# Optimization experiments

Measured on AMD Instinct MI355X. Metric: run time of the kernel, lower is better.

The kernel has to match this reference:

```python
import jax, jax.numpy as jnp
import numpy as np

T, B, IN, HID, NL = 256, 256, 64, 512, 2
LS = HID // NL  # per-layer hidden size of GRUCellStack


def setup_inputs() -> dict:
    key = jax.random.key(0)
    ks = jax.random.split(key, 9)
    w = lambda k, shape: (jax.random.normal(k, shape, jnp.float32) * 0.05)
    return {
        "obs": jax.random.normal(ks[0], (T, B, IN), jnp.float32),
        "reset": jax.random.randint(ks[1], (T, B), 0, 2).astype(bool),
        "h": jnp.zeros((B, HID), jnp.float32),
        "W_lin": w(ks[2], (HID, IN)),
        "b_lin": jnp.zeros((HID,), jnp.float32),
        "w_ih0": w(ks[3], (3 * LS, HID)),
        "w_hh0": w(ks[4], (3 * LS, LS)),
        "b_ih0": jnp.zeros((3 * LS,), jnp.float32),
        "b_hh0": jnp.zeros((3 * LS,), jnp.float32),
        "w_ih1": w(ks[5], (3 * LS, LS)),
        "w_hh1": w(ks[6], (3 * LS, LS)),
        "b_ih1": jnp.zeros((3 * LS,), jnp.float32),
        "b_hh1": jnp.zeros((3 * LS,), jnp.float32),
    }


def _gru_cell(i_gates, h, w_hh, b_hh):
    # PyTorch nn.GRUCell math; i_gates = x @ w_ih.T + b_ih precomputed.
    h_gates = h @ w_hh.T + b_hh
    ir, iz, in_ = jnp.split(i_gates, 3, axis=-1)
    hr, hz, hn = jnp.split(h_gates, 3, axis=-1)
    r = jax.nn.sigmoid(ir + hr)
    z = jax.nn.sigmoid(iz + hz)
    n = jnp.tanh(in_ + r * hn)
    return (1.0 - z) * n + z * h


def reference(obs, reset, h, W_lin, b_lin, w_ih0, w_hh0, b_ih0, b_hh0,
              w_ih1, w_hh1, b_ih1, b_hh1):
    # embed all timesteps at once: [T,B,HID]
    x = obs.astype(jnp.float32) @ W_lin.T + b_lin
    # layer-0 input-side gates depend only on x -> precompute: [T,B,3*LS]
    ig0 = x @ w_ih0.T + b_ih0
    mask = (~reset).astype(jnp.float32)[..., None]  # [T,B,1]

    def step(hc, inp):
        ig0_t, m_t = inp
        hc = hc * m_t                      # reset masking of full stacked state
        h0, h1 = jnp.split(hc, 2, axis=-1)  # per-layer states [B,LS]
        h0n = _gru_cell(ig0_t, h0, w_hh0, b_hh0)
        ig1 = h0n @ w_ih1.T + b_ih1
        h1n = _gru_cell(ig1, h1, w_hh1, b_hh1)
        hn = jnp.concatenate([h0n, h1n], axis=-1)  # [B,HID]
        return hn, hn

    _, states_h = jax.lax.scan(step, h, (ig0, mask))
    return states_h  # [T,B,HID]
```

## Files before the change

### kernel.cpp

```cpp
#include <hip/hip_runtime.h>

#define T_    256
#define B_    256
#define IN_   64
#define HID_  512
#define LS_   256
#define G3_   768
#define TBS_  32
#define MBT_  64
#define WP_   264
#define FSTRIDE_ 128

typedef short bf16x8v __attribute__((ext_vector_type(8)));
typedef float f32x4  __attribute__((ext_vector_type(4)));
typedef unsigned long long u64;

#define MFMA_B16(A, B, C) __builtin_amdgcn_mfma_f32_16x16x32_bf16(A, B, C, 0, 0, 0)

__device__ __forceinline__ unsigned short f2bf(float f) {
  union { float f; unsigned u; } v; v.f = f;
  unsigned r = v.u + 0x7fffu + ((v.u >> 16) & 1u);
  return (unsigned short)(r >> 16);
}
__device__ __forceinline__ float sigm(float x) { return 1.0f / (1.0f + __expf(-x)); }
__device__ __forceinline__ float tanh_f(float x) {
  x = fminf(fmaxf(x, -15.0f), 15.0f);
  float e = __expf(-2.0f * x);
  return (1.0f - e) / (1.0f + e);
}

__device__ __forceinline__ void st2_coh(unsigned short* p, unsigned short v) {
  __hip_atomic_store(p, v, __ATOMIC_RELAXED, __HIP_MEMORY_SCOPE_AGENT);
}
__device__ __forceinline__ bf16x8v ld16_coh(const unsigned short* p) {
  union { u64 q[2]; bf16x8v v; } u;
  u.q[0] = __hip_atomic_load((const u64*)p,     __ATOMIC_RELAXED, __HIP_MEMORY_SCOPE_AGENT);
  u.q[1] = __hip_atomic_load((const u64*)(p+4), __ATOMIC_RELAXED, __HIP_MEMORY_SCOPE_AGENT);
  return u.v;
}

__global__ void prep_conv(const float* __restrict__ whh0, const float* __restrict__ wih1,
                          const float* __restrict__ whh1, const unsigned char* __restrict__ rst,
                          unsigned short* __restrict__ dst, int* __restrict__ flagp,
                          int* __restrict__ flags) {
  const int idx = blockIdx.x * blockDim.x + threadIdx.x;
  const int N1 = G3_ * LS_;
  if (idx < 3 * N1) {
    float v;
    if (idx < N1)            v = whh0[idx];
    else if (idx < 2 * N1)   v = wih1[idx - N1];
    else                     v = whh1[idx - 2 * N1];
    dst[idx] = f2bf(v);
  }
  if (blockIdx.x == 1 && threadIdx.x < 32) {
    flags[threadIdx.x * FSTRIDE_] = 0;
  }
  if (blockIdx.x == 0) {
    __shared__ int f;
    if (threadIdx.x == 0) f = 0;
    __syncthreads();
    int any = 0;
    for (int i = 0; i < 8; ++i) {
      int off = threadIdx.x * 8 + i;
      if ((off & 3) && rst[off]) any = 1;
    }
    if (any) atomicOr(&f, 1);
    __syncthreads();
    if (threadIdx.x == 0) *flagp = f;
  }
}

__global__ void prep_wc(const float* __restrict__ W_lin, const float* __restrict__ b_lin,
                        const float* __restrict__ w_ih0, const float* __restrict__ b_ih0,
                        unsigned short* __restrict__ wc, float* __restrict__ bc) {
  const int n = blockIdx.x;
  const int i = threadIdx.x;
  const float* wrow = w_ih0 + (size_t)n * HID_;
  float acc = 0.f;
  for (int h = 0; h < HID_; ++h) acc += wrow[h] * W_lin[h * IN_ + i];
  wc[n * IN_ + i] = f2bf(acc);
  float pb = 0.f;
  for (int h = i; h < HID_; h += 64) pb += wrow[h] * b_lin[h];
  __shared__ float red[64];
  red[i] = pb;
  __syncthreads();
  if (i == 0) {
    float s = 0.f;
    for (int k = 0; k < 64; ++k) s += red[k];
    bc[n] = s + b_ih0[n];
  }
}

__global__ __launch_bounds__(512, 2) void gru_main(
    const float* __restrict__ obs, const unsigned char* __restrict__ rst,
    const float* __restrict__ h_init,
    const unsigned short* __restrict__ wc,
    const unsigned short* __restrict__ whh0g,
    const unsigned short* __restrict__ wih1g, const unsigned short* __restrict__ whh1g,
    const float* __restrict__ bcp, const float* __restrict__ bhh0,
    const float* __restrict__ bih1, const float* __restrict__ bhh1,
    const int* __restrict__ flagp, int* __restrict__ flag0,
    unsigned short* __restrict__ hx0, unsigned short* __restrict__ hx1,
    float* __restrict__ out) {

  __shared__ __align__(16) unsigned short wlds[3 * 96 * WP_];
  __shared__ int s_sm[64];
  __shared__ int s_start_sh;

  const int tid  = threadIdx.x;
  const int lane = tid & 63;
  const int wave = tid >> 6;
  const int l15  = lane & 15;
  const int quad = lane >> 4;
  const int mt   = wave & 3;
  const int c16  = (wave >> 2) * 16;

  const int x  = blockIdx.x;
  const int cx = x & 7, m8 = x >> 3;
  const int j  = m8 & 7;
  const int team = cx * 4 + (m8 >> 3);
  const int bg = team & 3, tc = team >> 2;
  const int b0 = bg * MBT_, t0 = tc * TBS_;

  int* f0 = flag0 + team * FSTRIDE_;

  const int flag = *flagp;
#define RVAL(i) (rst[flag ? (i) : ((i) << 2)] != 0)

#pragma unroll
  for (int q = 0; q < 3; ++q) {
    const unsigned short* src = (q == 0) ? whh0g : (q == 1) ? wih1g : whh1g;
    for (int cid = tid; cid < 96 * 32; cid += 512) {
      int lr = cid >> 5, off8 = (cid & 31) * 8;
      int g = lr >> 5, cc = lr & 31;
      int grow = (g << 8) + (j << 5) + cc;
      *(f32x4*)&wlds[(q * 96 + lr) * WP_ + off8] =
          *(const f32x4*)&src[(size_t)grow * 256 + off8];
    }
  }

  const int colg = j * 32 + c16 + l15;
  const float b0r = bcp[colg] + bhh0[colg];
  const float b0z = bcp[256 + colg] + bhh0[256 + colg];
  const float b0i = bcp[512 + colg];
  const float b0h = bhh0[512 + colg];
  const float b1r = bih1[colg] + bhh1[colg];
  const float b1z = bih1[256 + colg] + bhh1[256 + colg];
  const float b1i = bih1[512 + colg];
  const float b1h = bhh1[512 + colg];

  if (tid < 64) {
    int s = 0;
    for (int tt = t0; tt >= 1; --tt) {
      if (RVAL(tt * B_ + b0 + tid)) { s = tt; break; }
    }
    s_sm[tid] = s;
  }
  __syncthreads();
  if (tid == 0) {
    int s = s_sm[0];
    for (int k = 1; k < 64; ++k) s = s < s_sm[k] ? s : s_sm[k];
    s_start_sh = s;
  }
  __syncthreads();
  const int s_start = s_start_sh;

  bf16x8v h0A[8], h1A[8];
  const bf16x8v z8 = {0, 0, 0, 0, 0, 0, 0, 0};
#pragma unroll
  for (int kc = 0; kc < 8; ++kc) { h0A[kc] = z8; h1A[kc] = z8; }
  float h0v[4] = {0.f, 0.f, 0.f, 0.f}, h1v[4] = {0.f, 0.f, 0.f, 0.f};
  if (s_start == 0) {
    const float* hrow = h_init + (size_t)(b0 + mt * 16 + l15) * HID_;
#pragma unroll
    for (int kc = 0; kc < 8; ++kc) {
      f32x4 u0 = *(const f32x4*)(hrow + kc * 32 + quad * 8);
      f32x4 u1 = *(const f32x4*)(hrow + kc * 32 + quad * 8 + 4);
      f32x4 v0 = *(const f32x4*)(hrow + 256 + kc * 32 + quad * 8);
      f32x4 v1 = *(const f32x4*)(hrow + 256 + kc * 32 + quad * 8 + 4);
      bf16x8v a, b;
#pragma unroll
      for (int e = 0; e < 4; ++e) {
        a[e] = (short)f2bf(u0[e]); a[4 + e] = (short)f2bf(u1[e]);
        b[e] = (short)f2bf(v0[e]); b[4 + e] = (short)f2bf(v1[e]);
      }
      h0A[kc] = a; h1A[kc] = b;
    }
#pragma unroll
    for (int r = 0; r < 4; ++r) {
      const int m = mt * 16 + quad * 4 + r;
      h0v[r] = h_init[(size_t)(b0 + m) * HID_ + colg];
      h1v[r] = h_init[(size_t)(b0 + m) * HID_ + 256 + colg];
    }
  }

  const unsigned short* wR0 = &wlds[(0 * 96 + 0 * 32 + c16 + l15) * WP_];
  const unsigned short* wZ0 = &wlds[(0 * 96 + 1 * 32 + c16 + l15) * WP_];
  const unsigned short* wN0 = &wlds[(0 * 96 + 2 * 32 + c16 + l15) * WP_];
  const unsigned short* iR1 = &wlds[(1 * 96 + 0 * 32 + c16 + l15) * WP_];
  const unsigned short* iZ1 = &wlds[(1 * 96 + 1 * 32 + c16 + l15) * WP_];
  const unsigned short* iN1 = &wlds[(1 * 96 + 2 * 32 + c16 + l15) * WP_];
  const unsigned short* hR1 = &wlds[(2 * 96 + 0 * 32 + c16 + l15) * WP_];
  const unsigned short* hZ1 = &wlds[(2 * 96 + 1 * 32 + c16 + l15) * WP_];
  const unsigned short* hN1 = &wlds[(2 * 96 + 2 * 32 + c16 + l15) * WP_];

  f32x4 ou0a, ou0b, ou1a, ou1b;
  {
    const float* po = obs + ((size_t)s_start * B_ + b0 + mt * 16 + l15) * IN_;
    ou0a = __builtin_nontemporal_load((const f32x4*)(po + quad * 8));
    ou0b = __builtin_nontemporal_load((const f32x4*)(po + quad * 8 + 4));
    ou1a = __builtin_nontemporal_load((const f32x4*)(po + 32 + quad * 8));
    ou1b = __builtin_nontemporal_load((const f32x4*)(po + 32 + quad * 8 + 4));
  }

  for (int t = s_start; t < t0 + TBS_; ++t) {
    const int  kk = t - s_start + 1;
    const bool wr = (t >= t0);
    const bool rs0 = RVAL(t * B_ + b0 + mt * 16 + l15);
    bool rse[4];
#pragma unroll
    for (int r = 0; r < 4; ++r) rse[r] = RVAL(t * B_ + b0 + mt * 16 + quad * 4 + r);

    f32x4 ar = {0.f, 0.f, 0.f, 0.f}, az = ar, ani = ar, anh = ar;
    {
#pragma unroll
      for (int kc = 0; kc < 2; ++kc) {
        f32x4 u0 = kc ? ou1a : ou0a;
        f32x4 u1 = kc ? ou1b : ou0b;
        bf16x8v oA;
#pragma unroll
        for (int e = 0; e < 4; ++e) { oA[e] = (short)f2bf(u0[e]); oA[4 + e] = (short)f2bf(u1[e]); }
        const size_t wo = (size_t)colg * 64 + kc * 32 + quad * 8;
        bf16x8v br = *(const bf16x8v*)&wc[wo];
        bf16x8v bz = *(const bf16x8v*)&wc[wo + (size_t)256 * 64];
        bf16x8v bn = *(const bf16x8v*)&wc[wo + (size_t)512 * 64];
        ar  = MFMA_B16(oA, br, ar);
        az  = MFMA_B16(oA, bz, az);
        ani = MFMA_B16(oA, bn, ani);
      }
    }
#pragma unroll
    for (int kc = 0; kc < 8; ++kc) {
      bf16x8v am = rs0 ? z8 : h0A[kc];
      const int o = kc * 32 + quad * 8;
      ar  = MFMA_B16(am, *(const bf16x8v*)&wR0[o], ar);
      az  = MFMA_B16(am, *(const bf16x8v*)&wZ0[o], az);
      anh = MFMA_B16(am, *(const bf16x8v*)&wN0[o], anh);
    }
    {
      unsigned short* hw = hx0 + ((size_t)team * 2 + (kk & 1)) * (MBT_ * 256);
#pragma unroll
      for (int r = 0; r < 4; ++r) {
        const int m = mt * 16 + quad * 4 + r;
        float rr = sigm(ar[r] + b0r);
        float zz = sigm(az[r] + b0z);
        float nn = tanh_f(ani[r] + b0i + rr * (anh[r] + b0h));
        float hp = rse[r] ? 0.f : h0v[r];
        float hv = (1.f - zz) * nn + zz * hp;
        h0v[r] = hv;
        st2_coh(hw + m * 256 + colg, f2bf(hv));
      }
    }
    __syncthreads();
    if (tid == 0) {
      __hip_atomic_fetch_add(f0, 1, __ATOMIC_RELAXED, __HIP_MEMORY_SCOPE_AGENT);
      int cap = 0;
      while (__hip_atomic_load(f0, __ATOMIC_RELAXED, __HIP_MEMORY_SCOPE_AGENT)
                 < 8 * kk && cap < (1 << 16)) { __builtin_amdgcn_s_sleep(2); ++cap; }
    }
    __syncthreads();
    {
      const unsigned short* hr0 =
          hx0 + ((size_t)team * 2 + (kk & 1)) * (MBT_ * 256) + (mt * 16 + l15) * 256;
#pragma unroll
      for (int kc = 0; kc < 8; ++kc)
        h0A[kc] = ld16_coh(hr0 + kc * 32 + quad * 8);
      if (kk >= 2) {
        const unsigned short* hr1 =
            hx1 + ((size_t)team * 2 + ((kk - 1) & 1)) * (MBT_ * 256) + (mt * 16 + l15) * 256;
#pragma unroll
        for (int kc = 0; kc < 8; ++kc)
          h1A[kc] = ld16_coh(hr1 + kc * 32 + quad * 8);
      }
    }
    if (wr) {
#pragma unroll
      for (int r = 0; r < 4; ++r) {
        const int m = mt * 16 + quad * 4 + r;
        __builtin_nontemporal_store(h0v[r], &out[((size_t)t * B_ + b0 + m) * HID_ + colg]);
      }
    }
    if (t - 1 >= t0) {
#pragma unroll
      for (int r = 0; r < 4; ++r) {
        const int m = mt * 16 + quad * 4 + r;
        __builtin_nontemporal_store(h1v[r],
            &out[((size_t)(t - 1) * B_ + b0 + m) * HID_ + 256 + colg]);
      }
    }
    {
      const int tn = (t + 1 < t0 + TBS_) ? t + 1 : t;
      const float* po = obs + ((size_t)tn * B_ + b0 + mt * 16 + l15) * IN_;
      ou0a = __builtin_nontemporal_load((const f32x4*)(po + quad * 8));
      ou0b = __builtin_nontemporal_load((const f32x4*)(po + quad * 8 + 4));
      ou1a = __builtin_nontemporal_load((const f32x4*)(po + 32 + quad * 8));
      ou1b = __builtin_nontemporal_load((const f32x4*)(po + 32 + quad * 8 + 4));
    }

    ar = (f32x4){0.f, 0.f, 0.f, 0.f}; az = ar; ani = ar; anh = ar;
#pragma unroll
    for (int kc = 0; kc < 8; ++kc) {
      bf16x8v ai_ = h0A[kc];
      bf16x8v am  = rs0 ? z8 : h1A[kc];
      const int o = kc * 32 + quad * 8;
      ar  = MFMA_B16(ai_, *(const bf16x8v*)&iR1[o], ar);
      az  = MFMA_B16(ai_, *(const bf16x8v*)&iZ1[o], az);
      ani = MFMA_B16(ai_, *(const bf16x8v*)&iN1[o], ani);
      ar  = MFMA_B16(am, *(const bf16x8v*)&hR1[o], ar);
      az  = MFMA_B16(am, *(const bf16x8v*)&hZ1[o], az);
      anh = MFMA_B16(am, *(const bf16x8v*)&hN1[o], anh);
    }
    {
      unsigned short* hw = hx1 + ((size_t)team * 2 + (kk & 1)) * (MBT_ * 256);
#pragma unroll
      for (int r = 0; r < 4; ++r) {
        const int m = mt * 16 + quad * 4 + r;
        float rr = sigm(ar[r] + b1r);
        float zz = sigm(az[r] + b1z);
        float nn = tanh_f(ani[r] + b1i + rr * (anh[r] + b1h));
        float hp = rse[r] ? 0.f : h1v[r];
        float hv = (1.f - zz) * nn + zz * hp;
        h1v[r] = hv;
        st2_coh(hw + m * 256 + colg, f2bf(hv));
      }
    }
  }
  {
    const int tl = t0 + TBS_ - 1;
#pragma unroll
    for (int r = 0; r < 4; ++r) {
      const int m = mt * 16 + quad * 4 + r;
      __builtin_nontemporal_store(h1v[r],
          &out[((size_t)tl * B_ + b0 + m) * HID_ + 256 + colg]);
    }
  }
#undef RVAL
}

extern "C" void kernel_launch(void* const* d_in, const int* in_sizes, int n_in,
                              void* d_out, int out_size, void* d_ws, size_t ws_size,
                              hipStream_t stream) {
  const float* obs    = (const float*)d_in[0];
  const unsigned char* rst = (const unsigned char*)d_in[1];
  const float* h_init = (const float*)d_in[2];
  const float* W_lin  = (const float*)d_in[3];
  const float* b_lin  = (const float*)d_in[4];
  const float* w_ih0  = (const float*)d_in[5];
  const float* w_hh0  = (const float*)d_in[6];
  const float* b_ih0  = (const float*)d_in[7];
  const float* b_hh0  = (const float*)d_in[8];
  const float* w_ih1  = (const float*)d_in[9];
  const float* w_hh1  = (const float*)d_in[10];
  const float* b_ih1  = (const float*)d_in[11];
  const float* b_hh1  = (const float*)d_in[12];

  char* w = (char*)d_ws;
  unsigned short* wcp   = (unsigned short*)(w);
  unsigned short* whh0b = (unsigned short*)(w + 98304);
  unsigned short* wih1b = (unsigned short*)(w + 491520);
  unsigned short* whh1b = (unsigned short*)(w + 884736);
  float*          bcp   = (float*)(w + 1277952);
  int*            flagp = (int*)(w + 1281024);
  int*            flags = (int*)(w + 1281088);
  unsigned short* hx0   = (unsigned short*)(w + 1310720);
  unsigned short* hx1   = (unsigned short*)(w + 1310720 + 2097152);

  prep_conv<<<1152, 512, 0, stream>>>(w_hh0, w_ih1, w_hh1, rst, whh0b, flagp, flags);
  prep_wc<<<768, 64, 0, stream>>>(W_lin, b_lin, w_ih0, b_ih0, wcp, bcp);
  gru_main<<<256, 512, 0, stream>>>(obs, rst, h_init, wcp, whh0b, wih1b, whh1b,
                                    bcp, b_hh0, b_ih1, b_hh1, flagp,
                                    flags, hx0, hx1, (float*)d_out);
}
```

Measured before the change: 658.2 us.

## Rebalance GRU teams to 128-row batches with 16-step chunks, merge prep kernels

Each team now owns 128 batch rows over 16 time steps instead of 64 rows over 32 steps. Each wave covers one 16-row M tile and both 16-column groups, so every h-row A fragment is reused across two column groups. The intent is to shorten each team's sequential time chunk and its warm-up replay. The cost is more accumulators and registers per wave and larger exchange buffers. The two preprocessing kernels are merged into one launch, and the bias reduction now uses wave shuffles.

```diff
diff --git a/kernel.cpp b/kernel.cpp
--- a/kernel.cpp
+++ b/kernel.cpp
@@ -6,8 +6,8 @@
 #define HID_  512
 #define LS_   256
 #define G3_   768
-#define TBS_  32
-#define MBT_  64
+#define TBS_  16
+#define MBT_  128
 #define WP_   264
 #define FSTRIDE_ 128
 
@@ -39,55 +39,51 @@
   return u.v;
 }
 
-__global__ void prep_conv(const float* __restrict__ whh0, const float* __restrict__ wih1,
-                          const float* __restrict__ whh1, const unsigned char* __restrict__ rst,
-                          unsigned short* __restrict__ dst, int* __restrict__ flagp,
-                          int* __restrict__ flags) {
-  const int idx = blockIdx.x * blockDim.x + threadIdx.x;
-  const int N1 = G3_ * LS_;
-  if (idx < 3 * N1) {
-    float v;
-    if (idx < N1)            v = whh0[idx];
-    else if (idx < 2 * N1)   v = wih1[idx - N1];
-    else                     v = whh1[idx - 2 * N1];
-    dst[idx] = f2bf(v);
-  }
-  if (blockIdx.x == 1 && threadIdx.x < 32) {
-    flags[threadIdx.x * FSTRIDE_] = 0;
-  }
-  if (blockIdx.x == 0) {
-    __shared__ int f;
-    if (threadIdx.x == 0) f = 0;
-    __syncthreads();
-    int any = 0;
-    for (int i = 0; i < 8; ++i) {
-      int off = threadIdx.x * 8 + i;
-      if ((off & 3) && rst[off]) any = 1;
-    }
-    if (any) atomicOr(&f, 1);
-    __syncthreads();
-    if (threadIdx.x == 0) *flagp = f;
-  }
-}
-
-__global__ void prep_wc(const float* __restrict__ W_lin, const float* __restrict__ b_lin,
-                        const float* __restrict__ w_ih0, const float* __restrict__ b_ih0,
-                        unsigned short* __restrict__ wc, float* __restrict__ bc) {
-  const int n = blockIdx.x;
-  const int i = threadIdx.x;
-  const float* wrow = w_ih0 + (size_t)n * HID_;
-  float acc = 0.f;
-  for (int h = 0; h < HID_; ++h) acc += wrow[h] * W_lin[h * IN_ + i];
-  wc[n * IN_ + i] = f2bf(acc);
-  float pb = 0.f;
-  for (int h = i; h < HID_; h += 64) pb += wrow[h] * b_lin[h];
-  __shared__ float red[64];
-  red[i] = pb;
-  __syncthreads();
-  if (i == 0) {
-    float s = 0.f;
-    for (int k = 0; k < 64; ++k) s += red[k];
-    bc[n] = s + b_ih0[n];
+__global__ void prep_all(const float* __restrict__ whh0, const float* __restrict__ wih1,
+                         const float* __restrict__ whh1, const unsigned char* __restrict__ rst,
+                         const float* __restrict__ W_lin, const float* __restrict__ b_lin,
+                         const float* __restrict__ w_ih0, const float* __restrict__ b_ih0,
+                         unsigned short* __restrict__ dst, unsigned short* __restrict__ wc,
+                         float* __restrict__ bc, int* __restrict__ flagp,
+                         int* __restrict__ flags) {
+  const int bx = blockIdx.x;
+  const int tid = threadIdx.x;
+  if (bx < 1152) {
+    const int idx = bx * 512 + tid;
+    const int N1 = G3_ * LS_;
+    if (idx < 3 * N1) {
+      float v;
+      if (idx < N1)            v = whh0[idx];
+      else if (idx < 2 * N1)   v = wih1[idx - N1];
+      else                     v = whh1[idx - 2 * N1];
+      dst[idx] = f2bf(v);
+    }
+    if (bx == 1 && tid < 32) flags[tid * FSTRIDE_] = 0;
+    if (bx == 0) {
+      __shared__ int f;
+      if (tid == 0) f = 0;
+      __syncthreads();
+      int any = 0;
+      for (int i = 0; i < 8; ++i) {
+        int off = tid * 8 + i;
+        if ((off & 3) && rst[off]) any = 1;
+      }
+      if (any) atomicOr(&f, 1);
+      __syncthreads();
+      if (tid == 0) *flagp = f;
+    }
+  } else {
+    const int n = (bx - 1152) * 8 + (tid >> 6);
+    const int i = tid & 63;
+    const float* wrow = w_ih0 + (size_t)n * HID_;
+    float acc = 0.f;
+    for (int h = 0; h < HID_; ++h) acc += wrow[h] * W_lin[h * IN_ + i];
+    wc[n * IN_ + i] = f2bf(acc);
+    float pb = 0.f;
+    for (int h = i; h < HID_; h += 64) pb += wrow[h] * b_lin[h];
+#pragma unroll
+    for (int off = 32; off > 0; off >>= 1) pb += __shfl_down(pb, off);
+    if (i == 0) bc[n] = pb + b_ih0[n];
   }
 }
 
@@ -104,22 +100,20 @@
     float* __restrict__ out) {
 
   __shared__ __align__(16) unsigned short wlds[3 * 96 * WP_];
-  __shared__ int s_sm[64];
+  __shared__ int s_sm[128];
   __shared__ int s_start_sh;
 
   const int tid  = threadIdx.x;
   const int lane = tid & 63;
-  const int wave = tid >> 6;
+  const int w    = tid >> 6;
   const int l15  = lane & 15;
   const int quad = lane >> 4;
-  const int mt   = wave & 3;
-  const int c16  = (wave >> 2) * 16;
 
   const int x  = blockIdx.x;
   const int cx = x & 7, m8 = x >> 3;
   const int j  = m8 & 7;
   const int team = cx * 4 + (m8 >> 3);
-  const int bg = team & 3, tc = team >> 2;
+  const int bg = team & 1, tc = team >> 1;
   const int b0 = bg * MBT_, t0 = tc * TBS_;
 
   int* f0 = flag0 + team * FSTRIDE_;
@@ -139,17 +133,21 @@
     }
   }
 
-  const int colg = j * 32 + c16 + l15;
-  const float b0r = bcp[colg] + bhh0[colg];
-  const float b0z = bcp[256 + colg] + bhh0[256 + colg];
-  const float b0i = bcp[512 + colg];
-  const float b0h = bhh0[512 + colg];
-  const float b1r = bih1[colg] + bhh1[colg];
-  const float b1z = bih1[256 + colg] + bhh1[256 + colg];
-  const float b1i = bih1[512 + colg];
-  const float b1h = bhh1[512 + colg];
-
-  if (tid < 64) {
+  float b0r[2], b0z[2], b0i[2], b0h[2], b1r[2], b1z[2], b1i[2], b1h[2];
+#pragma unroll
+  for (int cg = 0; cg < 2; ++cg) {
+    const int c = j * 32 + cg * 16 + l15;
+    b0r[cg] = bcp[c] + bhh0[c];
+    b0z[cg] = bcp[256 + c] + bhh0[256 + c];
+    b0i[cg] = bcp[512 + c];
+    b0h[cg] = bhh0[512 + c];
+    b1r[cg] = bih1[c] + bhh1[c];
+    b1z[cg] = bih1[256 + c] + bhh1[256 + c];
+    b1i[cg] = bih1[512 + c];
+    b1h[cg] = bhh1[512 + c];
+  }
+
+  if (tid < 128) {
     int s = 0;
     for (int tt = t0; tt >= 1; --tt) {
       if (RVAL(tt * B_ + b0 + tid)) { s = tt; break; }
@@ -159,7 +157,7 @@
   __syncthreads();
   if (tid == 0) {
     int s = s_sm[0];
-    for (int k = 1; k < 64; ++k) s = s < s_sm[k] ? s : s_sm[k];
+    for (int k = 1; k < 128; ++k) s = s < s_sm[k] ? s : s_sm[k];
     s_start_sh = s;
   }
   __syncthreads();
@@ -169,9 +167,13 @@
   const bf16x8v z8 = {0, 0, 0, 0, 0, 0, 0, 0};
 #pragma unroll
   for (int kc = 0; kc < 8; ++kc) { h0A[kc] = z8; h1A[kc] = z8; }
-  float h0v[4] = {0.f, 0.f, 0.f, 0.f}, h1v[4] = {0.f, 0.f, 0.f, 0.f};
+  float h0v[2][4] = {{0.f}}, h1v[2][4] = {{0.f}};
+#pragma unroll
+  for (int cg = 0; cg < 2; ++cg)
+#pragma unroll
+    for (int r = 0; r < 4; ++r) { h0v[cg][r] = 0.f; h1v[cg][r] = 0.f; }
   if (s_start == 0) {
-    const float* hrow = h_init + (size_t)(b0 + mt * 16 + l15) * HID_;
+    const float* hrow = h_init + (size_t)(b0 + w * 16 + l15) * HID_;
 #pragma unroll
     for (int kc = 0; kc < 8; ++kc) {
       f32x4 u0 = *(const f32x4*)(hrow + kc * 32 + quad * 8);
@@ -187,26 +189,30 @@
       h0A[kc] = a; h1A[kc] = b;
     }
 #pragma unroll
-    for (int r = 0; r < 4; ++r) {
-      const int m = mt * 16 + quad * 4 + r;
-      h0v[r] = h_init[(size_t)(b0 + m) * HID_ + colg];
-      h1v[r] = h_init[(size_t)(b0 + m) * HID_ + 256 + colg];
-    }
-  }
-
-  const unsigned short* wR0 = &wlds[(0 * 96 + 0 * 32 + c16 + l15) * WP_];
-  const unsigned short* wZ0 = &wlds[(0 * 96 + 1 * 32 + c16 + l15) * WP_];
-  const unsigned short* wN0 = &wlds[(0 * 96 + 2 * 32 + c16 + l15) * WP_];
-  const unsigned short* iR1 = &wlds[(1 * 96 + 0 * 32 + c16 + l15) * WP_];
-  const unsigned short* iZ1 = &wlds[(1 * 96 + 1 * 32 + c16 + l15) * WP_];
-  const unsigned short* iN1 = &wlds[(1 * 96 + 2 * 32 + c16 + l15) * WP_];
-  const unsigned short* hR1 = &wlds[(2 * 96 + 0 * 32 + c16 + l15) * WP_];
-  const unsigned short* hZ1 = &wlds[(2 * 96 + 1 * 32 + c16 + l15) * WP_];
-  const unsigned short* hN1 = &wlds[(2 * 96 + 2 * 32 + c16 + l15) * WP_];
+    for (int cg = 0; cg < 2; ++cg)
+#pragma unroll
+      for (int r = 0; r < 4; ++r) {
+        const int m = w * 16 + quad * 4 + r;
+        const int c = j * 32 + cg * 16 + l15;
+        h0v[cg][r] = h_init[(size_t)(b0 + m) * HID_ + c];
+        h1v[cg][r] = h_init[(size_t)(b0 + m) * HID_ + 256 + c];
+      }
+  }
+
+  const unsigned short* wR0 = &wlds[(0 * 96 + 0 * 32 + l15) * WP_];
+  const unsigned short* wZ0 = &wlds[(0 * 96 + 1 * 32 + l15) * WP_];
+  const unsigned short* wN0 = &wlds[(0 * 96 + 2 * 32 + l15) * WP_];
+  const unsigned short* iR1 = &wlds[(1 * 96 + 0 * 32 + l15) * WP_];
+  const unsigned short* iZ1 = &wlds[(1 * 96 + 1 * 32 + l15) * WP_];
+  const unsigned short* iN1 = &wlds[(1 * 96 + 2 * 32 + l15) * WP_];
+  const unsigned short* hR1 = &wlds[(2 * 96 + 0 * 32 + l15) * WP_];
+  const unsigned short* hZ1 = &wlds[(2 * 96 + 1 * 32 + l15) * WP_];
+  const unsigned short* hN1 = &wlds[(2 * 96 + 2 * 32 + l15) * WP_];
+#define CGO_ (16 * WP_)
 
   f32x4 ou0a, ou0b, ou1a, ou1b;
   {
-    const float* po = obs + ((size_t)s_start * B_ + b0 + mt * 16 + l15) * IN_;
+    const float* po = obs + ((size_t)s_start * B_ + b0 + w * 16 + l15) * IN_;
     ou0a = __builtin_nontemporal_load((const f32x4*)(po + quad * 8));
     ou0b = __builtin_nontemporal_load((const f32x4*)(po + quad * 8 + 4));
     ou1a = __builtin_nontemporal_load((const f32x4*)(po + 32 + quad * 8));
@@ -216,12 +222,17 @@
   for (int t = s_start; t < t0 + TBS_; ++t) {
     const int  kk = t - s_start + 1;
     const bool wr = (t >= t0);
-    const bool rs0 = RVAL(t * B_ + b0 + mt * 16 + l15);
+    const bool rs0 = RVAL(t * B_ + b0 + w * 16 + l15);
     bool rse[4];
 #pragma unroll
-    for (int r = 0; r < 4; ++r) rse[r] = RVAL(t * B_ + b0 + mt * 16 + quad * 4 + r);
-
-    f32x4 ar = {0.f, 0.f, 0.f, 0.f}, az = ar, ani = ar, anh = ar;
+    for (int r = 0; r < 4; ++r) rse[r] = RVAL(t * B_ + b0 + w * 16 + quad * 4 + r);
+
+    f32x4 ar[2], az[2], ani[2], anh[2];
+#pragma unroll
+    for (int cg = 0; cg < 2; ++cg) {
+      ar[cg] = (f32x4){0.f, 0.f, 0.f, 0.f};
+      az[cg] = ar[cg]; ani[cg] = ar[cg]; anh[cg] = ar[cg];
+    }
     {
 #pragma unroll
       for (int kc = 0; kc < 2; ++kc) {
@@ -230,36 +241,44 @@
         bf16x8v oA;
 #pragma unroll
         for (int e = 0; e < 4; ++e) { oA[e] = (short)f2bf(u0[e]); oA[4 + e] = (short)f2bf(u1[e]); }
-        const size_t wo = (size_t)colg * 64 + kc * 32 + quad * 8;
-        bf16x8v br = *(const bf16x8v*)&wc[wo];
-        bf16x8v bz = *(const bf16x8v*)&wc[wo + (size_t)256 * 64];
-        bf16x8v bn = *(const bf16x8v*)&wc[wo + (size_t)512 * 64];
-        ar  = MFMA_B16(oA, br, ar);
-        az  = MFMA_B16(oA, bz, az);
-        ani = MFMA_B16(oA, bn, ani);
+#pragma unroll
+        for (int cg = 0; cg < 2; ++cg) {
+          const size_t wo = (size_t)(j * 32 + cg * 16 + l15) * 64 + kc * 32 + quad * 8;
+          bf16x8v br = *(const bf16x8v*)&wc[wo];
+          bf16x8v bz = *(const bf16x8v*)&wc[wo + (size_t)256 * 64];
+          bf16x8v bn = *(const bf16x8v*)&wc[wo + (size_t)512 * 64];
+          ar[cg]  = MFMA_B16(oA, br, ar[cg]);
+          az[cg]  = MFMA_B16(oA, bz, az[cg]);
+          ani[cg] = MFMA_B16(oA, bn, ani[cg]);
+        }
       }
     }
 #pragma unroll
     for (int kc = 0; kc < 8; ++kc) {
       bf16x8v am = rs0 ? z8 : h0A[kc];
       const int o = kc * 32 + quad * 8;
-      ar  = MFMA_B16(am, *(const bf16x8v*)&wR0[o], ar);
-      az  = MFMA_B16(am, *(const bf16x8v*)&wZ0[o], az);
-      anh = MFMA_B16(am, *(const bf16x8v*)&wN0[o], anh);
+#pragma unroll
+      for (int cg = 0; cg < 2; ++cg) {
+        ar[cg]  = MFMA_B16(am, *(const bf16x8v*)&wR0[o + cg * CGO_], ar[cg]);
+        az[cg]  = MFMA_B16(am, *(const bf16x8v*)&wZ0[o + cg * CGO_], az[cg]);
+        anh[cg] = MFMA_B16(am, *(const bf16x8v*)&wN0[o + cg * CGO_], anh[cg]);
+      }
     }
     {
       unsigned short* hw = hx0 + ((size_t)team * 2 + (kk & 1)) * (MBT_ * 256);
 #pragma unroll
-      for (int r = 0; r < 4; ++r) {
-        const int m = mt * 16 + quad * 4 + r;
-        float rr = sigm(ar[r] + b0r);
-        float zz = sigm(az[r] + b0z);
-        float nn = tanh_f(ani[r] + b0i + rr * (anh[r] + b0h));
-        float hp = rse[r] ? 0.f : h0v[r];
-        float hv = (1.f - zz) * nn + zz * hp;
-        h0v[r] = hv;
-        st2_coh(hw + m * 256 + colg, f2bf(hv));
-      }
+      for (int cg = 0; cg < 2; ++cg)
+#pragma unroll
+        for (int r = 0; r < 4; ++r) {
+          const int m = w * 16 + quad * 4 + r;
+          float rr = sigm(ar[cg][r] + b0r[cg]);
+          float zz = sigm(az[cg][r] + b0z[cg]);
+          float nn = tanh_f(ani[cg][r] + b0i[cg] + rr * (anh[cg][r] + b0h[cg]));
+          float hp = rse[r] ? 0.f : h0v[cg][r];
+          float hv = (1.f - zz) * nn + zz * hp;
+          h0v[cg][r] = hv;
+          st2_coh(hw + m * 256 + j * 32 + cg * 16 + l15, f2bf(hv));
+        }
     }
     __syncthreads();
     if (tid == 0) {
@@ -271,13 +290,13 @@
     __syncthreads();
     {
       const unsigned short* hr0 =
-          hx0 + ((size_t)team * 2 + (kk & 1)) * (MBT_ * 256) + (mt * 16 + l15) * 256;
+          hx0 + ((size_t)team * 2 + (kk & 1)) * (MBT_ * 256) + (w * 16 + l15) * 256;
 #pragma unroll
       for (int kc = 0; kc < 8; ++kc)
         h0A[kc] = ld16_coh(hr0 + kc * 32 + quad * 8);
       if (kk >= 2) {
         const unsigned short* hr1 =
-            hx1 + ((size_t)team * 2 + ((kk - 1) & 1)) * (MBT_ * 256) + (mt * 16 + l15) * 256;
+            hx1 + ((size_t)team * 2 + ((kk - 1) & 1)) * (MBT_ * 256) + (w * 16 + l15) * 256;
 #pragma unroll
         for (int kc = 0; kc < 8; ++kc)
           h1A[kc] = ld16_coh(hr1 + kc * 32 + quad * 8);
@@ -285,66 +304,83 @@
     }
     if (wr) {
 #pragma unroll
-      for (int r = 0; r < 4; ++r) {
-        const int m = mt * 16 + quad * 4 + r;
-        __builtin_nontemporal_store(h0v[r], &out[((size_t)t * B_ + b0 + m) * HID_ + colg]);
-      }
+      for (int cg = 0; cg < 2; ++cg)
+#pragma unroll
+        for (int r = 0; r < 4; ++r) {
+          const int m = w * 16 + quad * 4 + r;
+          __builtin_nontemporal_store(h0v[cg][r],
+              &out[((size_t)t * B_ + b0 + m) * HID_ + j * 32 + cg * 16 + l15]);
+        }
     }
     if (t - 1 >= t0) {
 #pragma unroll
-      for (int r = 0; r < 4; ++r) {
-        const int m = mt * 16 + quad * 4 + r;
-        __builtin_nontemporal_store(h1v[r],
-            &out[((size_t)(t - 1) * B_ + b0 + m) * HID_ + 256 + colg]);
-      }
+      for (int cg = 0; cg < 2; ++cg)
+#pragma unroll
+        for (int r = 0; r < 4; ++r) {
+          const int m = w * 16 + quad * 4 + r;
+          __builtin_nontemporal_store(h1v[cg][r],
+              &out[((size_t)(t - 1) * B_ + b0 + m) * HID_ + 256 + j * 32 + cg * 16 + l15]);
+        }
     }
     {
       const int tn = (t + 1 < t0 + TBS_) ? t + 1 : t;
-      const float* po = obs + ((size_t)tn * B_ + b0 + mt * 16 + l15) * IN_;
+      const float* po = obs + ((size_t)tn * B_ + b0 + w * 16 + l15) * IN_;
       ou0a = __builtin_nontemporal_load((const f32x4*)(po + quad * 8));
       ou0b = __builtin_nontemporal_load((const f32x4*)(po + quad * 8 + 4));
       ou1a = __builtin_nontemporal_load((const f32x4*)(po + 32 + quad * 8));
       ou1b = __builtin_nontemporal_load((const f32x4*)(po + 32 + quad * 8 + 4));
     }
 
-    ar = (f32x4){0.f, 0.f, 0.f, 0.f}; az = ar; ani = ar; anh = ar;
+#pragma unroll
+    for (int cg = 0; cg < 2; ++cg) {
+      ar[cg] = (f32x4){0.f, 0.f, 0.f, 0.f};
+      az[cg] = ar[cg]; ani[cg] = ar[cg]; anh[cg] = ar[cg];
+    }
 #pragma unroll
     for (int kc = 0; kc < 8; ++kc) {
       bf16x8v ai_ = h0A[kc];
       bf16x8v am  = rs0 ? z8 : h1A[kc];
       const int o = kc * 32 + quad * 8;
-      ar  = MFMA_B16(ai_, *(const bf16x8v*)&iR1[o], ar);
-      az  = MFMA_B16(ai_, *(const bf16x8v*)&iZ1[o], az);
-      ani = MFMA_B16(ai_, *(const bf16x8v*)&iN1[o], ani);
-      ar  = MFMA_B16(am, *(const bf16x8v*)&hR1[o], ar);
-      az  = MFMA_B16(am, *(const bf16x8v*)&hZ1[o], az);
-      anh = MFMA_B16(am, *(const bf16x8v*)&hN1[o], anh);
+#pragma unroll
+      for (int cg = 0; cg < 2; ++cg) {
+        ar[cg]  = MFMA_B16(ai_, *(const bf16x8v*)&iR1[o + cg * CGO_], ar[cg]);
+        az[cg]  = MFMA_B16(ai_, *(const bf16x8v*)&iZ1[o + cg * CGO_], az[cg]);
+        ani[cg] = MFMA_B16(ai_, *(const bf16x8v*)&iN1[o + cg * CGO_], ani[cg]);
+        ar[cg]  = MFMA_B16(am, *(const bf16x8v*)&hR1[o + cg * CGO_], ar[cg]);
+        az[cg]  = MFMA_B16(am, *(const bf16x8v*)&hZ1[o + cg * CGO_], az[cg]);
+        anh[cg] = MFMA_B16(am, *(const bf16x8v*)&hN1[o + cg * CGO_], anh[cg]);
+      }
     }
     {
       unsigned short* hw = hx1 + ((size_t)team * 2 + (kk & 1)) * (MBT_ * 256);
 #pragma unroll
-      for (int r = 0; r < 4; ++r) {
-        const int m = mt * 16 + quad * 4 + r;
-        float rr = sigm(ar[r] + b1r);
-        float zz = sigm(az[r] + b1z);
-        float nn = tanh_f(ani[r] + b1i + rr * (anh[r] + b1h));
-        float hp = rse[r] ? 0.f : h1v[r];
-        float hv = (1.f - zz) * nn + zz * hp;
-        h1v[r] = hv;
-        st2_coh(hw + m * 256 + colg, f2bf(hv));
-      }
+      for (int cg = 0; cg < 2; ++cg)
+#pragma unroll
+        for (int r = 0; r < 4; ++r) {
+          const int m = w * 16 + quad * 4 + r;
+          float rr = sigm(ar[cg][r] + b1r[cg]);
+          float zz = sigm(az[cg][r] + b1z[cg]);
+          float nn = tanh_f(ani[cg][r] + b1i[cg] + rr * (anh[cg][r] + b1h[cg]));
+          float hp = rse[r] ? 0.f : h1v[cg][r];
+          float hv = (1.f - zz) * nn + zz * hp;
+          h1v[cg][r] = hv;
+          st2_coh(hw + m * 256 + j * 32 + cg * 16 + l15, f2bf(hv));
+        }
     }
   }
   {
     const int tl = t0 + TBS_ - 1;
 #pragma unroll
-    for (int r = 0; r < 4; ++r) {
-      const int m = mt * 16 + quad * 4 + r;
-      __builtin_nontemporal_store(h1v[r],
-          &out[((size_t)tl * B_ + b0 + m) * HID_ + 256 + colg]);
-    }
+    for (int cg = 0; cg < 2; ++cg)
+#pragma unroll
+      for (int r = 0; r < 4; ++r) {
+        const int m = w * 16 + quad * 4 + r;
+        __builtin_nontemporal_store(h1v[cg][r],
+            &out[((size_t)tl * B_ + b0 + m) * HID_ + 256 + j * 32 + cg * 16 + l15]);
+      }
   }
 #undef RVAL
+#undef CGO_
 }
 
 extern "C" void kernel_launch(void* const* d_in, const int* in_sizes, int n_in,
@@ -373,10 +409,11 @@
   int*            flagp = (int*)(w + 1281024);
   int*            flags = (int*)(w + 1281088);
   unsigned short* hx0   = (unsigned short*)(w + 1310720);
-  unsigned short* hx1   = (unsigned short*)(w + 1310720 + 2097152);
-
-  prep_conv<<<1152, 512, 0, stream>>>(w_hh0, w_ih1, w_hh1, rst, whh0b, flagp, flags);
-  prep_wc<<<768, 64, 0, stream>>>(W_lin, b_lin, w_ih0, b_ih0, wcp, bcp);
+  unsigned short* hx1   = (unsigned short*)(w + 1310720 + 4194304);
+
+  prep_all<<<1152 + 96, 512, 0, stream>>>(w_hh0, w_ih1, w_hh1, rst,
+                                          W_lin, b_lin, w_ih0, b_ih0,
+                                          whh0b, wcp, bcp, flagp, flags);
   gru_main<<<256, 512, 0, stream>>>(obs, rst, h_init, wcp, whh0b, wih1b, whh1b,
                                     bcp, b_hh0, b_ih1, b_hh1, flagp,
                                     flags, hx0, hx1, (float*)d_out);
```

New measurement: 655.4 us. No clear change (-0.4%).
